# Performance work log

Hardware: AMD Instinct MI355X
Metric: run time of the kernel (lower is better)

The kernel has to match this reference:

```python
import jax, jax.numpy as jnp
import numpy as np

B, V, H, NI, E = 512, 50, 768, 8, 2


def setup_inputs() -> dict:
    key = jax.random.key(0)
    ks = jax.random.split(key, 8)
    s1 = 1.0 / np.sqrt(2 * H)
    s = 1.0 / np.sqrt(H)
    return {
        "variable_states": jax.random.normal(ks[0], (B, V, H), jnp.float32),
        "edge_probs": jax.random.uniform(ks[1], (B, V, V, E), jnp.float32),
        "intervention_values": jax.random.normal(ks[2], (B, NI, H), jnp.float32),
        "W1": jax.random.normal(ks[3], (2 * H, H), jnp.float32) * s1,
        "b1": jnp.zeros((H,), jnp.float32),
        "W2": jax.random.normal(ks[4], (H, H), jnp.float32) * s,
        "b2": jnp.zeros((H,), jnp.float32),
        "Wg1": jax.random.normal(ks[5], (H, H), jnp.float32) * s,
        "bg1": jnp.zeros((H,), jnp.float32),
        "Wg2": jax.random.normal(ks[6], (H, 1), jnp.float32) * s,
        "bg2": jnp.zeros((1,), jnp.float32),
        "intervention_indices": jax.random.randint(ks[7], (B, NI), 0, V, jnp.int64),
    }


def _do_operator(variable_states, intervention_values, intervention_indices,
                 W1, b1, W2, b2, Wg1, bg1, Wg2, bg2):
    idx = intervention_indices                              # [B, NI]
    valid = (idx >= 0) & (idx < V)                          # [B, NI]
    idx_c = jnp.clip(idx, 0, V - 1)
    # gather all original vars for every intervention at once: [B, NI, H]
    orig = jnp.take_along_axis(variable_states, idx_c[..., None], axis=1)
    x = jnp.concatenate([orig, intervention_values], axis=-1)      # [B, NI, 2H]
    enc = jax.nn.gelu(x @ W1 + b1, approximate=False) @ W2 + b2    # [B, NI, H]
    gate = jax.nn.sigmoid(
        jax.nn.gelu(enc @ Wg1 + bg1, approximate=False) @ Wg2 + bg2
    )                                                              # [B, NI, 1]
    blended = orig * (1.0 - gate) + intervention_values * gate     # [B, NI, H]
    states = variable_states
    b_ar = jnp.arange(B)
    for i in range(NI):
        cur = states[b_ar, idx_c[:, i]]                            # [B, H]
        new = jnp.where(valid[:, i, None], blended[:, i], cur)
        states = states.at[b_ar, idx_c[:, i]].set(new)
    return states


def reference(variable_states, edge_probs, intervention_values,
              W1, b1, W2, b2, Wg1, bg1, Wg2, bg2, intervention_indices):
    # edge_probs is mutated in-place in the torch original but not returned;
    # the returned value is only the intervened states.
    return _do_operator(variable_states, intervention_values, intervention_indices,
                        W1, b1, W2, b2, Wg1, bg1, Wg2, bg2)
```

## Files before the change

### kernel.cpp

```cpp
#include <hip/hip_runtime.h>
#include <math.h>

#define B_  512
#define V_  50
#define H_  768
#define NI_ 8
#define M_  (B_ * NI_)
#define K1_ (2 * H_)
#define NCB_ 12
#define NGEMM_ 384
#define NCOPY_ 256
#define COPY_PER_BLK_ 6400

using f32x4 = __attribute__((ext_vector_type(4))) float;
using s16x8 = __attribute__((ext_vector_type(8))) short;

__device__ __forceinline__ float gelu_exact(float x) {
    return 0.5f * x * (1.0f + erff(x * 0.7071067811865476f));
}

__device__ __forceinline__ short f2bf(float f) {
    union { float f; unsigned u; } v; v.f = f;
    unsigned r = (v.u + 0x7fffu + ((v.u >> 16) & 1u)) >> 16;
    return (short)r;
}

#define GLOAD16(g, l)                                                          \
    __builtin_amdgcn_global_load_lds(                                          \
        (const __attribute__((address_space(1))) void*)(g),                    \
        (__attribute__((address_space(3))) void*)(l), 16, 0, 0)

__global__ __launch_bounds__(256) void pre_kernel(
    const float* __restrict__ vs, const float* __restrict__ iv,
    const int* __restrict__ idx,
    const float* __restrict__ W1, const float* __restrict__ W2,
    const float* __restrict__ Wg1,
    short* __restrict__ W1t, short* __restrict__ W2t, short* __restrict__ Wg1t,
    short* __restrict__ X) {
    __shared__ short s[64][65];
    const int blk = blockIdx.x;
    const int tid = threadIdx.x;

    if (blk < 576) {
        const float* src; short* dst; int K, t;
        if (blk < 288)      { src = W1;  dst = W1t;  K = K1_; t = blk; }
        else if (blk < 432) { src = W2;  dst = W2t;  K = H_;  t = blk - 288; }
        else                { src = Wg1; dst = Wg1t; K = H_;  t = blk - 432; }
        int bx = t % 12, by = t / 12;
        int k0 = by * 64, n0 = bx * 64;
#pragma unroll
        for (int e = 0; e < 16; ++e) {
            int li = tid + e * 256;
            int kk = li >> 6, nn = li & 63;
            s[kk][nn] = f2bf(src[(size_t)(k0 + kk) * H_ + n0 + nn]);
        }
        __syncthreads();
#pragma unroll
        for (int e = 0; e < 16; ++e) {
            int li = tid + e * 256;
            int nn = li >> 6, kk = li & 63;
            dst[(size_t)(n0 + nn) * K + k0 + kk] = s[kk][nn];
        }
    } else {
        int g = blk - 576;
        int r = g * 4 + (tid >> 6);
        int lane = tid & 63;
        int b = r >> 3;
        int id = idx[r];
        id = min(max(id, 0), V_ - 1);
        const float4* s1 = (const float4*)(vs + ((size_t)b * V_ + id) * H_);
        const float4* s2 = (const float4*)(iv + (size_t)r * H_);
        short* xr = X + (size_t)r * K1_;
#pragma unroll
        for (int part = 0; part < 3; ++part) {
            int e = lane + part * 64;
            float4 a = s1[e];
            float4 c = s2[e];
            short4 oa, oc;
            oa.x = f2bf(a.x); oa.y = f2bf(a.y); oa.z = f2bf(a.z); oa.w = f2bf(a.w);
            oc.x = f2bf(c.x); oc.y = f2bf(c.y); oc.z = f2bf(c.z); oc.w = f2bf(c.w);
            *(short4*)&xr[e * 4] = oa;
            *(short4*)&xr[H_ + e * 4] = oc;
        }
    }
}

__device__ __forceinline__ short* lds_ptr(short* base, int row, int byteoff) {
    return (short*)((char*)base + row * 128 + (byteoff ^ ((row & 7) << 4)));
}

template <int ACT, int GATE>
__global__ __launch_bounds__(256) void gemm_mfma(
    const short* __restrict__ A,
    const short* __restrict__ Bt,
    const float* __restrict__ bias,
    short* __restrict__ C,
    int M, int N, int K,
    const float* __restrict__ wg2, float* __restrict__ gate_part,
    const float4* __restrict__ cpy_src, float4* __restrict__ cpy_dst,
    size_t cpy_base) {
    __shared__ short As[2][128 * 64];
    __shared__ short Bs[2][64 * 64];

    const int tid = threadIdx.x;
    const int bid = blockIdx.x;

    if (bid >= NGEMM_) {
        size_t base = cpy_base + (size_t)(bid - NGEMM_) * COPY_PER_BLK_;
#pragma unroll 5
        for (int e = 0; e < COPY_PER_BLK_ / 256; ++e) {
            size_t i = base + (size_t)e * 256 + tid;
            cpy_dst[i] = cpy_src[i];
        }
        return;
    }

    const int lane = tid & 63;
    const int wave = tid >> 6;
    const int llo = lane & 15;
    const int lhi = lane >> 4;

    int sw = (bid & 7) * 48 + (bid >> 3);
    int bx = sw % 12, by = sw / 12;
    const int row0 = by * 128;
    const int col0 = bx * 64;

    const short* gsrc[6];
    short* ldst0[6];
    int lstep[6];
#pragma unroll
    for (int p = 0; p < 6; ++p) {
        int c = wave * 6 + p;
        int jj = lane & 7;
        if (c < 16) {
            int r = c * 8 + (lane >> 3);
            int j = jj ^ (r & 7);
            gsrc[p] = A + (size_t)(row0 + r) * K + j * 8;
            ldst0[p] = &As[0][c * 512];
            lstep[p] = 128 * 64;
        } else {
            int r = (c - 16) * 8 + (lane >> 3);
            int j = jj ^ (r & 7);
            gsrc[p] = Bt + (size_t)(col0 + r) * K + j * 8;
            ldst0[p] = &Bs[0][(c - 16) * 512];
            lstep[p] = 64 * 64;
        }
    }

    f32x4 acc[2][4];
#pragma unroll
    for (int mi = 0; mi < 2; ++mi)
#pragma unroll
        for (int nf = 0; nf < 4; ++nf) acc[mi][nf] = (f32x4){0, 0, 0, 0};

    const int nt = K >> 6;
#pragma unroll
    for (int p = 0; p < 6; ++p) GLOAD16(gsrc[p], ldst0[p]);
    __syncthreads();

    for (int t = 0; t < nt; ++t) {
        const int cur = t & 1;
        if (t + 1 < nt) {
#pragma unroll
            for (int p = 0; p < 6; ++p)
                GLOAD16(gsrc[p] + (size_t)(t + 1) * 64,
                        ldst0[p] + (cur ^ 1) * lstep[p]);
        }
        short* Ab = (short*)As[cur];
        short* Bb = (short*)Bs[cur];
#pragma unroll
        for (int ks = 0; ks < 2; ++ks) {
            s16x8 a[2], b[4];
#pragma unroll
            for (int mi = 0; mi < 2; ++mi)
                a[mi] = *(const s16x8*)lds_ptr(Ab, wave * 32 + mi * 16 + llo,
                                               ks * 64 + lhi * 16);
#pragma unroll
            for (int nf = 0; nf < 4; ++nf)
                b[nf] = *(const s16x8*)lds_ptr(Bb, nf * 16 + llo,
                                               ks * 64 + lhi * 16);
#pragma unroll
            for (int mi = 0; mi < 2; ++mi)
#pragma unroll
                for (int nf = 0; nf < 4; ++nf)
                    acc[mi][nf] = __builtin_amdgcn_mfma_f32_16x16x32_bf16(
                        a[mi], b[nf], acc[mi][nf], 0, 0, 0);
        }
        __syncthreads();
    }

    if (!GATE) {
#pragma unroll
        for (int nf = 0; nf < 4; ++nf) {
            int cc = col0 + nf * 16 + llo;
            float bv = bias[cc];
#pragma unroll
            for (int mi = 0; mi < 2; ++mi) {
#pragma unroll
                for (int j = 0; j < 4; ++j) {
                    int rr = row0 + wave * 32 + mi * 16 + lhi * 4 + j;
                    float v = acc[mi][nf][j] + bv;
                    if (ACT) v = gelu_exact(v);
                    C[(size_t)rr * N + cc] = f2bf(v);
                }
            }
        }
    } else {
        float s[2][4];
#pragma unroll
        for (int mi = 0; mi < 2; ++mi)
#pragma unroll
            for (int j = 0; j < 4; ++j) s[mi][j] = 0.f;
#pragma unroll
        for (int nf = 0; nf < 4; ++nf) {
            int cc = col0 + nf * 16 + llo;
            float bv = bias[cc];
            float wv = wg2[cc];
#pragma unroll
            for (int mi = 0; mi < 2; ++mi)
#pragma unroll
                for (int j = 0; j < 4; ++j)
                    s[mi][j] += gelu_exact(acc[mi][nf][j] + bv) * wv;
        }
#pragma unroll
        for (int off = 1; off < 16; off <<= 1)
#pragma unroll
            for (int mi = 0; mi < 2; ++mi)
#pragma unroll
                for (int j = 0; j < 4; ++j)
                    s[mi][j] += __shfl_xor(s[mi][j], off);
        if (llo == 0) {
#pragma unroll
            for (int mi = 0; mi < 2; ++mi)
#pragma unroll
                for (int j = 0; j < 4; ++j) {
                    int rr = row0 + wave * 32 + mi * 16 + lhi * 4 + j;
                    gate_part[(size_t)rr * NCB_ + bx] = s[mi][j];
                }
        }
    }
}

__global__ __launch_bounds__(192) void final_blend(
    const float* __restrict__ vs, const float* __restrict__ iv,
    const int* __restrict__ idx, const float* __restrict__ gate_part,
    const float* __restrict__ bg2, float* __restrict__ out) {
    int r = blockIdx.x;
    int b = r >> 3, i = r & 7;
    int id = idx[r];
    if (id < 0 || id >= V_) return;
    for (int j = i + 1; j < NI_; ++j)
        if (idx[b * NI_ + j] == id) return;
    __shared__ float gsh;
    if (threadIdx.x == 0) {
        float s = bg2[0];
#pragma unroll
        for (int c = 0; c < NCB_; ++c) s += gate_part[(size_t)r * NCB_ + c];
        gsh = 1.f / (1.f + expf(-s));
    }
    __syncthreads();
    float g = gsh;
    int t = threadIdx.x;
    const float4* src = (const float4*)(vs + ((size_t)b * V_ + id) * H_);
    const float4* ivr = (const float4*)(iv + (size_t)r * H_);
    float4* dst = (float4*)(out + ((size_t)b * V_ + id) * H_);
    float4 o = src[t], x = ivr[t], res;
    res.x = o.x * (1.f - g) + x.x * g;
    res.y = o.y * (1.f - g) + x.y * g;
    res.z = o.z * (1.f - g) + x.z * g;
    res.w = o.w * (1.f - g) + x.w * g;
    dst[t] = res;
}

extern "C" void kernel_launch(void* const* d_in, const int* in_sizes, int n_in,
                              void* d_out, int out_size, void* d_ws, size_t ws_size,
                              hipStream_t stream) {
    const float* vs  = (const float*)d_in[0];
    const float* iv  = (const float*)d_in[2];
    const float* W1  = (const float*)d_in[3];
    const float* b1  = (const float*)d_in[4];
    const float* W2  = (const float*)d_in[5];
    const float* b2  = (const float*)d_in[6];
    const float* Wg1 = (const float*)d_in[7];
    const float* bg1 = (const float*)d_in[8];
    const float* Wg2 = (const float*)d_in[9];
    const float* bg2 = (const float*)d_in[10];
    const int*   idx = (const int*)d_in[11];
    float* out = (float*)d_out;

    char* ws = (char*)d_ws;
    short* Xb   = (short*)ws;
    short* encb = Xb;
    short* h1b  = (short*)(ws + (size_t)M_ * K1_ * 2);
    float* gate_part = (float*)(ws + (size_t)M_ * K1_ * 2 + (size_t)M_ * H_ * 2);
    short* W1t  = (short*)((char*)gate_part + (size_t)M_ * NCB_ * 4);
    short* W2t  = W1t + (size_t)H_ * K1_;
    short* Wg1t = W2t + (size_t)H_ * H_;

    const float4* cs = (const float4*)vs;
    float4* cd = (float4*)out;
    const size_t CHUNK = (size_t)NCOPY_ * COPY_PER_BLK_;

    pre_kernel<<<1600, 256, 0, stream>>>(vs, iv, idx, W1, W2, Wg1,
                                         W1t, W2t, Wg1t, Xb);

    const int nblk = NGEMM_ + NCOPY_;
    gemm_mfma<1, 0><<<nblk, 256, 0, stream>>>(Xb, W1t, b1, h1b, M_, H_, K1_,
                                              nullptr, nullptr, cs, cd, 0);
    gemm_mfma<0, 0><<<nblk, 256, 0, stream>>>(h1b, W2t, b2, encb, M_, H_, H_,
                                              nullptr, nullptr, cs, cd, CHUNK);
    gemm_mfma<1, 1><<<nblk, 256, 0, stream>>>(encb, Wg1t, bg1, nullptr, M_, H_, H_,
                                              Wg2, gate_part, cs, cd, 2 * CHUNK);
    final_blend<<<M_, 192, 0, stream>>>(vs, iv, idx, gate_part, bg2, out);
}
```

Before: 81.36 us.

## Fold W2 into gate weight matrix to drop one activation GEMM

Because enc = h1@W2 + b2 feeds only the gate, the code precomputes Wc = W2@Wg1 (as a small GEMM on weights) and bc = b2@Wg1 + bg1, so the gate GEMM runs directly on h1. This removes the 4096x768x768 activation GEMM and one kernel launch, with the weight-product GEMM run alongside the first GEMM and part of the state copy. It adds bf16 rounding of the fused weight product, which changes numerics slightly, and rebalances the output copy across two launches.

New measurement: 75.44 us. -7.3%, faster.

```diff
diff --git a/kernel.cpp b/kernel.cpp
--- a/kernel.cpp
+++ b/kernel.cpp
@@ -8,9 +8,8 @@
 #define M_  (B_ * NI_)
 #define K1_ (2 * H_)
 #define NCB_ 12
-#define NGEMM_ 384
-#define NCOPY_ 256
-#define COPY_PER_BLK_ 6400
+#define N4_     4915200
+#define SPLIT4_ 2949120
 
 using f32x4 = __attribute__((ext_vector_type(4))) float;
 using s16x8 = __attribute__((ext_vector_type(8))) short;
@@ -29,23 +28,27 @@
     __builtin_amdgcn_global_load_lds(                                          \
         (const __attribute__((address_space(1))) void*)(g),                    \
         (__attribute__((address_space(3))) void*)(l), 16, 0, 0)
+
+__device__ __forceinline__ short* lds_ptr(short* base, int row, int byteoff) {
+    return (short*)((char*)base + row * 128 + (byteoff ^ ((row & 7) << 4)));
+}
 
 __global__ __launch_bounds__(256) void pre_kernel(
     const float* __restrict__ vs, const float* __restrict__ iv,
     const int* __restrict__ idx,
     const float* __restrict__ W1, const float* __restrict__ W2,
     const float* __restrict__ Wg1,
-    short* __restrict__ W1t, short* __restrict__ W2t, short* __restrict__ Wg1t,
-    short* __restrict__ X) {
+    const float* __restrict__ b2, const float* __restrict__ bg1,
+    short* __restrict__ W1t, short* __restrict__ W2b, short* __restrict__ Wg1t,
+    short* __restrict__ X, float* __restrict__ bc) {
     __shared__ short s[64][65];
     const int blk = blockIdx.x;
     const int tid = threadIdx.x;
 
-    if (blk < 576) {
+    if (blk < 288 || (blk >= 432 && blk < 576)) {
         const float* src; short* dst; int K, t;
-        if (blk < 288)      { src = W1;  dst = W1t;  K = K1_; t = blk; }
-        else if (blk < 432) { src = W2;  dst = W2t;  K = H_;  t = blk - 288; }
-        else                { src = Wg1; dst = Wg1t; K = H_;  t = blk - 432; }
+        if (blk < 288) { src = W1;  dst = W1t;  K = K1_; t = blk; }
+        else           { src = Wg1; dst = Wg1t; K = H_;  t = blk - 432; }
         int bx = t % 12, by = t / 12;
         int k0 = by * 64, n0 = bx * 64;
 #pragma unroll
@@ -61,7 +64,17 @@
             int nn = li >> 6, kk = li & 63;
             dst[(size_t)(n0 + nn) * K + k0 + kk] = s[kk][nn];
         }
-    } else {
+    } else if (blk < 432) {
+        size_t base = (size_t)(blk - 288) * 4096;
+#pragma unroll
+        for (int e = 0; e < 4; ++e) {
+            size_t i = base + (size_t)e * 1024 + tid * 4;
+            float4 a = *(const float4*)(W2 + i);
+            short4 o;
+            o.x = f2bf(a.x); o.y = f2bf(a.y); o.z = f2bf(a.z); o.w = f2bf(a.w);
+            *(short4*)(W2b + i) = o;
+        }
+    } else if (blk < 1600) {
         int g = blk - 576;
         int r = g * 4 + (tid >> 6);
         int lane = tid & 63;
@@ -82,48 +95,31 @@
             *(short4*)&xr[e * 4] = oa;
             *(short4*)&xr[H_ + e * 4] = oc;
         }
-    }
-}
-
-__device__ __forceinline__ short* lds_ptr(short* base, int row, int byteoff) {
-    return (short*)((char*)base + row * 128 + (byteoff ^ ((row & 7) << 4)));
-}
-
-template <int ACT, int GATE>
-__global__ __launch_bounds__(256) void gemm_mfma(
-    const short* __restrict__ A,
-    const short* __restrict__ Bt,
-    const float* __restrict__ bias,
-    short* __restrict__ C,
-    int M, int N, int K,
-    const float* __restrict__ wg2, float* __restrict__ gate_part,
-    const float4* __restrict__ cpy_src, float4* __restrict__ cpy_dst,
-    size_t cpy_base) {
-    __shared__ short As[2][128 * 64];
-    __shared__ short Bs[2][64 * 64];
-
-    const int tid = threadIdx.x;
-    const int bid = blockIdx.x;
-
-    if (bid >= NGEMM_) {
-        size_t base = cpy_base + (size_t)(bid - NGEMM_) * COPY_PER_BLK_;
-#pragma unroll 5
-        for (int e = 0; e < COPY_PER_BLK_ / 256; ++e) {
-            size_t i = base + (size_t)e * 256 + tid;
-            cpy_dst[i] = cpy_src[i];
-        }
-        return;
-    }
-
+    } else {
+        __shared__ float part[4][64];
+        int c = blk - 1600;
+        int sub = tid >> 6;
+        int jj = tid & 63;
+        int j = c * 64 + jj;
+        float sum = 0.f;
+        for (int k = sub * 192; k < sub * 192 + 192; ++k)
+            sum += b2[k] * Wg1[(size_t)k * H_ + j];
+        part[sub][jj] = sum;
+        __syncthreads();
+        if (sub == 0)
+            bc[j] = part[0][jj] + part[1][jj] + part[2][jj] + part[3][jj] + bg1[j];
+    }
+}
+
+__device__ __forceinline__ void gemm_body(
+    const short* __restrict__ A, const short* __restrict__ Bt,
+    const float* __restrict__ bias, short* __restrict__ C,
+    int N, int K, int act, int row0, int col0,
+    short (*As)[128 * 64], short (*Bs)[64 * 64], int tid) {
     const int lane = tid & 63;
     const int wave = tid >> 6;
     const int llo = lane & 15;
     const int lhi = lane >> 4;
-
-    int sw = (bid & 7) * 48 + (bid >> 3);
-    int bx = sw % 12, by = sw / 12;
-    const int row0 = by * 128;
-    const int col0 = bx * 64;
 
     const short* gsrc[6];
     short* ldst0[6];
@@ -189,55 +185,173 @@
         __syncthreads();
     }
 
-    if (!GATE) {
-#pragma unroll
-        for (int nf = 0; nf < 4; ++nf) {
-            int cc = col0 + nf * 16 + llo;
-            float bv = bias[cc];
-#pragma unroll
-            for (int mi = 0; mi < 2; ++mi) {
-#pragma unroll
-                for (int j = 0; j < 4; ++j) {
-                    int rr = row0 + wave * 32 + mi * 16 + lhi * 4 + j;
-                    float v = acc[mi][nf][j] + bv;
-                    if (ACT) v = gelu_exact(v);
-                    C[(size_t)rr * N + cc] = f2bf(v);
-                }
+#pragma unroll
+    for (int nf = 0; nf < 4; ++nf) {
+        int cc = col0 + nf * 16 + llo;
+        float bv = bias ? bias[cc] : 0.0f;
+#pragma unroll
+        for (int mi = 0; mi < 2; ++mi) {
+#pragma unroll
+            for (int j = 0; j < 4; ++j) {
+                int rr = row0 + wave * 32 + mi * 16 + lhi * 4 + j;
+                float v = acc[mi][nf][j] + bv;
+                if (act) v = gelu_exact(v);
+                C[(size_t)rr * N + cc] = f2bf(v);
             }
         }
+    }
+}
+
+__global__ __launch_bounds__(256) void mega1(
+    const short* __restrict__ Xb, const short* __restrict__ W1t,
+    const float* __restrict__ b1, short* __restrict__ h1b,
+    const short* __restrict__ Wg1t, const short* __restrict__ W2b,
+    short* __restrict__ Wct,
+    const float4* __restrict__ cs, float4* __restrict__ cd) {
+    __shared__ short As[2][128 * 64];
+    __shared__ short Bs[2][64 * 64];
+    const int bid = blockIdx.x;
+    const int tid = threadIdx.x;
+
+    if (bid < 384) {
+        int sw = (bid & 7) * 48 + (bid >> 3);
+        int bx = sw % 12, by = sw / 12;
+        gemm_body(Xb, W1t, b1, h1b, H_, K1_, 1, by * 128, bx * 64, As, Bs, tid);
+    } else if (bid < 456) {
+        int t = bid - 384;
+        int bx = t % 12, by = t / 12;
+        gemm_body(Wg1t, W2b, nullptr, Wct, H_, H_, 0, by * 128, bx * 64, As, Bs, tid);
     } else {
-        float s[2][4];
+        int lb = bid - 456;
+        for (size_t i = (size_t)lb * 256 + tid; i < (size_t)SPLIT4_;
+             i += (size_t)184 * 256)
+            cd[i] = cs[i];
+    }
+}
+
+__global__ __launch_bounds__(256) void gate_gemm(
+    const short* __restrict__ h1b, const short* __restrict__ Wct,
+    const float* __restrict__ bc, const float* __restrict__ wg2,
+    float* __restrict__ gate_part,
+    const float4* __restrict__ cs, float4* __restrict__ cd) {
+    __shared__ short As[2][128 * 64];
+    __shared__ short Bs[2][64 * 64];
+    const int bid = blockIdx.x;
+    const int tid = threadIdx.x;
+
+    if (bid >= 384) {
+        int lb = bid - 384;
+        for (size_t i = (size_t)SPLIT4_ + (size_t)lb * 256 + tid; i < (size_t)N4_;
+             i += (size_t)256 * 256)
+            cd[i] = cs[i];
+        return;
+    }
+
+    const int lane = tid & 63;
+    const int wave = tid >> 6;
+    const int llo = lane & 15;
+    const int lhi = lane >> 4;
+    int sw = (bid & 7) * 48 + (bid >> 3);
+    int bx = sw % 12, by = sw / 12;
+    const int row0 = by * 128;
+    const int col0 = bx * 64;
+    const int K = H_;
+
+    const short* gsrc[6];
+    short* ldst0[6];
+    int lstep[6];
+#pragma unroll
+    for (int p = 0; p < 6; ++p) {
+        int c = wave * 6 + p;
+        int jj = lane & 7;
+        if (c < 16) {
+            int r = c * 8 + (lane >> 3);
+            int j = jj ^ (r & 7);
+            gsrc[p] = h1b + (size_t)(row0 + r) * K + j * 8;
+            ldst0[p] = &As[0][c * 512];
+            lstep[p] = 128 * 64;
+        } else {
+            int r = (c - 16) * 8 + (lane >> 3);
+            int j = jj ^ (r & 7);
+            gsrc[p] = Wct + (size_t)(col0 + r) * K + j * 8;
+            ldst0[p] = &Bs[0][(c - 16) * 512];
+            lstep[p] = 64 * 64;
+        }
+    }
+
+    f32x4 acc[2][4];
+#pragma unroll
+    for (int mi = 0; mi < 2; ++mi)
+#pragma unroll
+        for (int nf = 0; nf < 4; ++nf) acc[mi][nf] = (f32x4){0, 0, 0, 0};
+
+    const int nt = K >> 6;
+#pragma unroll
+    for (int p = 0; p < 6; ++p) GLOAD16(gsrc[p], ldst0[p]);
+    __syncthreads();
+
+    for (int t = 0; t < nt; ++t) {
+        const int cur = t & 1;
+        if (t + 1 < nt) {
+#pragma unroll
+            for (int p = 0; p < 6; ++p)
+                GLOAD16(gsrc[p] + (size_t)(t + 1) * 64,
+                        ldst0[p] + (cur ^ 1) * lstep[p]);
+        }
+        short* Ab = (short*)As[cur];
+        short* Bb = (short*)Bs[cur];
+#pragma unroll
+        for (int ks = 0; ks < 2; ++ks) {
+            s16x8 a[2], b[4];
+#pragma unroll
+            for (int mi = 0; mi < 2; ++mi)
+                a[mi] = *(const s16x8*)lds_ptr(Ab, wave * 32 + mi * 16 + llo,
+                                               ks * 64 + lhi * 16);
+#pragma unroll
+            for (int nf = 0; nf < 4; ++nf)
+                b[nf] = *(const s16x8*)lds_ptr(Bb, nf * 16 + llo,
+                                               ks * 64 + lhi * 16);
+#pragma unroll
+            for (int mi = 0; mi < 2; ++mi)
+#pragma unroll
+                for (int nf = 0; nf < 4; ++nf)
+                    acc[mi][nf] = __builtin_amdgcn_mfma_f32_16x16x32_bf16(
+                        a[mi], b[nf], acc[mi][nf], 0, 0, 0);
+        }
+        __syncthreads();
+    }
+
+    float s[2][4];
+#pragma unroll
+    for (int mi = 0; mi < 2; ++mi)
+#pragma unroll
+        for (int j = 0; j < 4; ++j) s[mi][j] = 0.f;
+#pragma unroll
+    for (int nf = 0; nf < 4; ++nf) {
+        int cc = col0 + nf * 16 + llo;
+        float bv = bc[cc];
+        float wv = wg2[cc];
 #pragma unroll
         for (int mi = 0; mi < 2; ++mi)
 #pragma unroll
-            for (int j = 0; j < 4; ++j) s[mi][j] = 0.f;
-#pragma unroll
-        for (int nf = 0; nf < 4; ++nf) {
-            int cc = col0 + nf * 16 + llo;
-            float bv = bias[cc];
-            float wv = wg2[cc];
-#pragma unroll
-            for (int mi = 0; mi < 2; ++mi)
-#pragma unroll
-                for (int j = 0; j < 4; ++j)
-                    s[mi][j] += gelu_exact(acc[mi][nf][j] + bv) * wv;
-        }
-#pragma unroll
-        for (int off = 1; off < 16; off <<= 1)
-#pragma unroll
-            for (int mi = 0; mi < 2; ++mi)
-#pragma unroll
-                for (int j = 0; j < 4; ++j)
-                    s[mi][j] += __shfl_xor(s[mi][j], off);
-        if (llo == 0) {
-#pragma unroll
-            for (int mi = 0; mi < 2; ++mi)
-#pragma unroll
-                for (int j = 0; j < 4; ++j) {
-                    int rr = row0 + wave * 32 + mi * 16 + lhi * 4 + j;
-                    gate_part[(size_t)rr * NCB_ + bx] = s[mi][j];
-                }
-        }
+            for (int j = 0; j < 4; ++j)
+                s[mi][j] += gelu_exact(acc[mi][nf][j] + bv) * wv;
+    }
+#pragma unroll
+    for (int off = 1; off < 16; off <<= 1)
+#pragma unroll
+        for (int mi = 0; mi < 2; ++mi)
+#pragma unroll
+            for (int j = 0; j < 4; ++j)
+                s[mi][j] += __shfl_xor(s[mi][j], off);
+    if (llo == 0) {
+#pragma unroll
+        for (int mi = 0; mi < 2; ++mi)
+#pragma unroll
+            for (int j = 0; j < 4; ++j) {
+                int rr = row0 + wave * 32 + mi * 16 + lhi * 4 + j;
+                gate_part[(size_t)rr * NCB_ + bx] = s[mi][j];
+            }
     }
 }
 
@@ -290,26 +404,20 @@
 
     char* ws = (char*)d_ws;
     short* Xb   = (short*)ws;
-    short* encb = Xb;
     short* h1b  = (short*)(ws + (size_t)M_ * K1_ * 2);
     float* gate_part = (float*)(ws + (size_t)M_ * K1_ * 2 + (size_t)M_ * H_ * 2);
     short* W1t  = (short*)((char*)gate_part + (size_t)M_ * NCB_ * 4);
-    short* W2t  = W1t + (size_t)H_ * K1_;
-    short* Wg1t = W2t + (size_t)H_ * H_;
+    short* W2b  = W1t + (size_t)H_ * K1_;
+    short* Wg1t = W2b + (size_t)H_ * H_;
+    short* Wct  = Wg1t + (size_t)H_ * H_;
+    float* bc   = (float*)(Wct + (size_t)H_ * H_);
 
     const float4* cs = (const float4*)vs;
     float4* cd = (float4*)out;
-    const size_t CHUNK = (size_t)NCOPY_ * COPY_PER_BLK_;
-
-    pre_kernel<<<1600, 256, 0, stream>>>(vs, iv, idx, W1, W2, Wg1,
-                                         W1t, W2t, Wg1t, Xb);
-
-    const int nblk = NGEMM_ + NCOPY_;
-    gemm_mfma<1, 0><<<nblk, 256, 0, stream>>>(Xb, W1t, b1, h1b, M_, H_, K1_,
-                                              nullptr, nullptr, cs, cd, 0);
-    gemm_mfma<0, 0><<<nblk, 256, 0, stream>>>(h1b, W2t, b2, encb, M_, H_, H_,
-                                              nullptr, nullptr, cs, cd, CHUNK);
-    gemm_mfma<1, 1><<<nblk, 256, 0, stream>>>(encb, Wg1t, bg1, nullptr, M_, H_, H_,
-                                              Wg2, gate_part, cs, cd, 2 * CHUNK);
+
+    pre_kernel<<<1612, 256, 0, stream>>>(vs, iv, idx, W1, W2, Wg1, b2, bg1,
+                                         W1t, W2b, Wg1t, Xb, bc);
+    mega1<<<640, 256, 0, stream>>>(Xb, W1t, b1, h1b, Wg1t, W2b, Wct, cs, cd);
+    gate_gemm<<<640, 256, 0, stream>>>(h1b, Wct, bc, Wg2, gate_part, cs, cd);
     final_blend<<<M_, 192, 0, stream>>>(vs, iv, idx, gate_part, bg2, out);
 }
```
